# Optimization experiments

Measured on AMD Instinct MI355X. Metric: run time of the kernel, lower is better.

Reference implementation:

```python
import jax, jax.numpy as jnp
import numpy as np

D_MODEL, N_HEADS, D_K, D_V = 1024, 16, 64, 64
B, S = 4, 2048
EPS = 1e-5


def setup_inputs() -> dict:
    key = jax.random.key(0)
    ks = jax.random.split(key, 8)
    scale = 1.0 / np.sqrt(D_MODEL)
    return {
        "input_Q": jax.random.normal(ks[0], (B, S, D_MODEL), dtype=jnp.float32),
        "input_K": jax.random.normal(ks[1], (B, S, D_MODEL), dtype=jnp.float32),
        "input_V": jax.random.normal(ks[2], (B, S, D_MODEL), dtype=jnp.float32),
        "attn_mask": jax.random.bernoulli(ks[3], 0.15, (B, S, S)),  # True = masked
        "W_Q": jax.random.uniform(ks[4], (N_HEADS * D_K, D_MODEL), jnp.float32, -scale, scale),
        "W_K": jax.random.uniform(ks[5], (N_HEADS * D_K, D_MODEL), jnp.float32, -scale, scale),
        "W_V": jax.random.uniform(ks[6], (N_HEADS * D_V, D_MODEL), jnp.float32, -scale, scale),
        "W_fc": jax.random.uniform(ks[7], (D_MODEL, N_HEADS * D_V), jnp.float32, -scale, scale),
    }


def _proj(x, W, h, d):
    # x: [B,S,D] @ W.T ([D, h*d]) -> [B,h,S,d]
    b, s, _ = x.shape
    y = jnp.einsum("bsd,ed->bse", x, W)
    return y.reshape(b, s, h, d).transpose(0, 2, 1, 3)


def reference(input_Q, input_K, input_V, attn_mask, W_Q, W_K, W_V, W_fc):
    b, s, d_model = input_Q.shape
    Q = _proj(input_Q, W_Q, N_HEADS, D_K)  # [B,H,S,dk]
    K = _proj(input_K, W_K, N_HEADS, D_K)
    V = _proj(input_V, W_V, N_HEADS, D_V)

    scores = jnp.einsum("bhqd,bhkd->bhqk", Q, K) / np.sqrt(D_K).astype(np.float32)
    scores = jnp.where(attn_mask[:, None, :, :], jnp.float32(-1e9), scores)
    attn = jax.nn.softmax(scores, axis=-1)  # [B,H,S,S]

    context = jnp.einsum("bhqk,bhkd->bhqd", attn, V)
    context = context.transpose(0, 2, 1, 3).reshape(b, s, N_HEADS * D_V)
    output = jnp.einsum("bse,de->bsd", context, W_fc)

    x = output + input_Q  # residual
    mu = jnp.mean(x, axis=-1, keepdims=True)
    var = jnp.mean(jnp.square(x - mu), axis=-1, keepdims=True)
    ln = (x - mu) / jnp.sqrt(var + EPS)  # fresh LayerNorm: gamma=1, beta=0
    return ln, attn
```

## Files before the change

### kernel.cpp

```cpp
#include <hip/hip_runtime.h>
#include <cstdint>
#include <cstddef>

constexpr int Bc  = 4;
constexpr int Sc  = 2048;
constexpr int DMc = 1024;
constexpr int Hc  = 16;
constexpr int DHc = 64;
constexpr int BHc = Bc * Hc;

typedef float f32x4  __attribute__((ext_vector_type(4)));
typedef short bf16x8 __attribute__((ext_vector_type(8)));

static __device__ __forceinline__ short f2bf(float x) {
  uint32_t u = __builtin_bit_cast(uint32_t, x);
  u += 0x7fffu + ((u >> 16) & 1u);
  return (short)(u >> 16);
}

static __device__ __forceinline__ f32x4 mfma16(bf16x8 a, bf16x8 b, f32x4 c) {
  return __builtin_amdgcn_mfma_f32_16x16x32_bf16(a, b, c, 0, 0, 0);
}

static __device__ __forceinline__ void gload16(const short* g, short* l) {
  __builtin_amdgcn_global_load_lds(
      (const __attribute__((address_space(1))) void*)g,
      (__attribute__((address_space(3))) void*)l, 16, 0, 0);
}

__global__ __launch_bounds__(256) void k_cvtall(const float* __restrict__ iQ,
                                                const float* __restrict__ iK,
                                                const float* __restrict__ iV,
                                                const float* __restrict__ wQ,
                                                const float* __restrict__ wK,
                                                const float* __restrict__ wV,
                                                const float* __restrict__ wO,
                                                short* __restrict__ oQ,
                                                short* __restrict__ oK,
                                                short* __restrict__ oV,
                                                short* __restrict__ owQ,
                                                short* __restrict__ owK,
                                                short* __restrict__ owV,
                                                short* __restrict__ owO) {
  const int bid = blockIdx.x;
  const float* in;
  short* out;
  int ib;
  if (bid < 8192)        { in = iQ; out = oQ; ib = bid; }
  else if (bid < 16384)  { in = iK; out = oK; ib = bid - 8192; }
  else if (bid < 24576)  { in = iV; out = oV; ib = bid - 16384; }
  else {
    const int wb = bid - 24576;
    const int sel = wb >> 10;
    in  = sel == 0 ? wQ : (sel == 1 ? wK : (sel == 2 ? wV : wO));
    out = sel == 0 ? owQ : (sel == 1 ? owK : (sel == 2 ? owV : owO));
    ib = wb & 1023;
  }
  const int i = ib * 256 + threadIdx.x;
  float4 v = reinterpret_cast<const float4*>(in)[i];
  short4 o;
  o.x = f2bf(v.x); o.y = f2bf(v.y); o.z = f2bf(v.z); o.w = f2bf(v.w);
  reinterpret_cast<short4*>(out)[i] = o;
}

template <int MODE>
static __device__ __forceinline__ void gemm_body(const short* __restrict__ A,
                                                 const short* __restrict__ Bt,
                                                 void* __restrict__ out,
                                                 int bm, int bn) {
  __shared__ __align__(16) short lA[128 * 64];
  __shared__ __align__(16) short lB[128 * 64];
  const int tid = threadIdx.x;
  const int lane = tid & 63, w = tid >> 6;
  const int wr = w >> 1, wc = w & 1;
  const int r = lane & 15, g = lane >> 4;

  const int lrow8 = lane >> 3;
  const int lsl   = lane & 7;

  f32x4 acc[4][4] = {};
  const short* Ab = A + (size_t)bm * DMc;
  const short* Bb = Bt + (size_t)bn * DMc;

  for (int k0 = 0; k0 < DMc; k0 += 64) {
    __syncthreads();
    #pragma unroll
    for (int rnd = 0; rnd < 4; rnd++) {
      const int row = rnd * 32 + w * 8 + lrow8;
      const int slot = lsl ^ (row & 7);
      gload16(Ab + (size_t)row * DMc + k0 + slot * 8, lA + (rnd * 32 + w * 8) * 64);
      gload16(Bb + (size_t)row * DMc + k0 + slot * 8, lB + (rnd * 32 + w * 8) * 64);
    }
    __syncthreads();

    #pragma unroll
    for (int kk = 0; kk < 2; kk++) {
      bf16x8 af[4], bfr[4];
      #pragma unroll
      for (int i = 0; i < 4; i++) {
        const int arow = wr * 64 + i * 16 + r;
        af[i] = *reinterpret_cast<const bf16x8*>(
            lA + arow * 64 + (((kk * 4 + g) ^ (arow & 7)) << 3));
        const int brow = wc * 64 + i * 16 + r;
        bfr[i] = *reinterpret_cast<const bf16x8*>(
            lB + brow * 64 + (((kk * 4 + g) ^ (brow & 7)) << 3));
      }
      #pragma unroll
      for (int i = 0; i < 4; i++)
        #pragma unroll
        for (int n = 0; n < 4; n++) acc[i][n] = mfma16(af[i], bfr[n], acc[i][n]);
    }
  }

  #pragma unroll
  for (int i = 0; i < 4; i++) {
    #pragma unroll
    for (int n = 0; n < 4; n++) {
      const int col = bn + wc * 64 + n * 16 + r;
      #pragma unroll
      for (int j = 0; j < 4; j++) {
        const int m = bm + wr * 64 + i * 16 + g * 4 + j;
        if (MODE == 2) {
          reinterpret_cast<float*>(out)[(size_t)m * DMc + col] = acc[i][n][j];
        } else {
          const int b = m >> 11, s = m & (Sc - 1);
          const int h = col >> 6, d = col & (DHc - 1);
          size_t idx = (MODE == 1)
              ? ((size_t)(b * Hc + h) * DHc + d) * Sc + s
              : ((size_t)(b * Hc + h) * Sc + s) * DHc + d;
          reinterpret_cast<short*>(out)[idx] = f2bf(acc[i][n][j]);
        }
      }
    }
  }
}

__global__ __launch_bounds__(256) void k_gemmQKV_pack(
    const short* __restrict__ XQ, const short* __restrict__ XK,
    const short* __restrict__ XV, const short* __restrict__ WQ,
    const short* __restrict__ WK, const short* __restrict__ WV,
    short* __restrict__ Q, short* __restrict__ K, short* __restrict__ V,
    const int* __restrict__ msk, uint32_t* __restrict__ bits) {
  const int bid = blockIdx.x;
  if (bid < 1536) {
    const int rem = bid & 511;
    const int bm = (rem & 63) * 128, bn = (rem >> 6) * 128;
    const int z = bid >> 9;
    if (z == 0)      gemm_body<0>(XQ, WQ, (void*)Q, bm, bn);
    else if (z == 1) gemm_body<0>(XK, WK, (void*)K, bm, bn);
    else             gemm_body<1>(XV, WV, (void*)V, bm, bn);
  } else {
    const size_t wi = (size_t)(bid - 1536) * 256 + threadIdx.x;
    const uint4* mp = reinterpret_cast<const uint4*>(msk + wi * 32);
    uint32_t word = 0;
    #pragma unroll
    for (int q = 0; q < 8; q++) {
      const uint4 mv = mp[q];
      word |= (mv.x != 0 ? 1u : 0u) << (q * 4 + 0);
      word |= (mv.y != 0 ? 1u : 0u) << (q * 4 + 1);
      word |= (mv.z != 0 ? 1u : 0u) << (q * 4 + 2);
      word |= (mv.w != 0 ? 1u : 0u) << (q * 4 + 3);
    }
    bits[wi] = word;
  }
}

__global__ __launch_bounds__(512, 4) void k_flash2(const short* __restrict__ Qb,
                                                   const short* __restrict__ Kb,
                                                   const short* __restrict__ Vt,
                                                   const uint32_t* __restrict__ pbits,
                                                   short* __restrict__ ctx,
                                                   float* __restrict__ attn) {
  __shared__ __align__(16) short kbuf[2][4096];
  __shared__ __align__(16) short vbuf[2][4096];
  __shared__ __align__(16) short pbuf[8][1024];

  const int lin = blockIdx.x;
  const int bh = (lin & 7) * 8 + (lin >> 7);
  const int qbase = ((lin >> 3) & 15) * 128;
  const int b = bh >> 4, h = bh & 15;
  const int tid = threadIdx.x;
  const int lane = tid & 63, w = tid >> 6;
  const int r = lane & 15, g = lane >> 4;
  const int rx = r & 7;

  const int srow = tid >> 3;
  const int sslot = (tid & 7) ^ (srow & 7);
  const short* ksrc = Kb + ((size_t)bh * Sc + srow) * DHc + sslot * 8;
  const short* vsrc = Vt + ((size_t)bh * DHc + srow) * Sc + sslot * 8;
  short* const kdst0 = &kbuf[0][w * 512];
  short* const kdst1 = &kbuf[1][w * 512];
  short* const vdst0 = &vbuf[0][w * 512];
  short* const vdst1 = &vbuf[1][w * 512];

  const short* qrow = Qb + ((size_t)bh * Sc + qbase + w * 16 + r) * DHc;
  const bf16x8 qf0 = *reinterpret_cast<const bf16x8*>(qrow + g * 8);
  const bf16x8 qf1 = *reinterpret_cast<const bf16x8*>(qrow + g * 8 + 32);

  const uint32_t* mrow = pbits + ((size_t)b * Sc + qbase + w * 16 + r) * (Sc / 32);

  constexpr float SCL = 0.18033688f;
  f32x4 pacc[4] = {};
  float rs = 0.f;

  gload16(ksrc, kdst0);
  gload16(vsrc, vdst0);
  __syncthreads();

  int cur = 0;
  for (int kt = 0; kt < 32; kt++) {
    if (kt + 1 < 32) {
      gload16(ksrc + (size_t)(kt + 1) * 64 * DHc, cur ? kdst0 : kdst1);
      gload16(vsrc + (kt + 1) * 64,               cur ? vdst0 : vdst1);
    }
    const short* kb = kbuf[cur];
    const short* vb = vbuf[cur];

    f32x4 sc4[4];
    #pragma unroll
    for (int tt = 0; tt < 4; tt++) {
      const int krow = (tt * 16 + r) * 64;
      bf16x8 kf0 = *reinterpret_cast<const bf16x8*>(kb + krow + ((g ^ rx) << 3));
      bf16x8 kf1 = *reinterpret_cast<const bf16x8*>(kb + krow + (((g + 4) ^ rx) << 3));
      f32x4 a = {};
      a = mfma16(kf0, qf0, a);
      a = mfma16(kf1, qf1, a);
      sc4[tt] = a;
    }

    const uint2 mu = *reinterpret_cast<const uint2*>(mrow + kt * 2);
    #pragma unroll
    for (int tt = 0; tt < 4; tt++) {
      const uint32_t mword = (tt < 2) ? mu.x : mu.y;
      const int bsh = (tt & 1) * 16 + g * 4;
      f32x4 e;
      #pragma unroll
      for (int j = 0; j < 4; j++) {
        float v = __builtin_exp2f(sc4[tt][j] * SCL);
        if ((mword >> (bsh + j)) & 1u) v = 0.f;
        e[j] = v;
        rs += v;
      }
      uint32_t lo = (uint32_t)(uint16_t)f2bf(e[0]) | ((uint32_t)(uint16_t)f2bf(e[1]) << 16);
      uint32_t hi = (uint32_t)(uint16_t)f2bf(e[2]) | ((uint32_t)(uint16_t)f2bf(e[3]) << 16);
      uint64_t pk = (uint64_t)lo | ((uint64_t)hi << 32);
      *reinterpret_cast<uint64_t*>(
          &pbuf[w][r * 64 + (((tt * 2 + (g >> 1)) ^ rx) << 3) + ((g & 1) << 2)]) = pk;
    }

    #pragma unroll
    for (int kt2 = 0; kt2 < 2; kt2++) {
      const int sl = ((kt2 * 4 + g) ^ rx) << 3;
      const bf16x8 paf = *reinterpret_cast<const bf16x8*>(&pbuf[w][r * 64 + sl]);
      #pragma unroll
      for (int n = 0; n < 4; n++) {
        const bf16x8 vf = *reinterpret_cast<const bf16x8*>(vb + (n * 16 + r) * 64 + sl);
        pacc[n] = mfma16(paf, vf, pacc[n]);
      }
    }

    __syncthreads();
    cur ^= 1;
  }

  rs += __shfl_xor(rs, 16);
  rs += __shfl_xor(rs, 32);
  const float rinv = 1.0f / rs;

  float riv[4];
  #pragma unroll
  for (int j = 0; j < 4; j++) riv[j] = 1.0f / __shfl(rs, g * 4 + j);

  short* cbase = ctx + ((size_t)b * Sc + qbase + w * 16) * DMc + h * DHc;
  #pragma unroll
  for (int n = 0; n < 4; n++)
    #pragma unroll
    for (int j = 0; j < 4; j++)
      cbase[(size_t)(g * 4 + j) * DMc + n * 16 + r] = f2bf(pacc[n][j] * riv[j]);

  const short* kbase = Kb + (size_t)bh * Sc * DHc;
  float* out = attn + ((size_t)bh * Sc + qbase + w * 16 + r) * Sc;
  #pragma unroll 2
  for (int kt = 0; kt < 32; kt++) {
    const uint2 mu = *reinterpret_cast<const uint2*>(mrow + kt * 2);
    #pragma unroll
    for (int tt = 0; tt < 4; tt++) {
      const short* krow = kbase + (size_t)(kt * 64 + tt * 16 + r) * DHc;
      bf16x8 kf0 = *reinterpret_cast<const bf16x8*>(krow + g * 8);
      bf16x8 kf1 = *reinterpret_cast<const bf16x8*>(krow + g * 8 + 32);
      f32x4 a = {};
      a = mfma16(kf0, qf0, a);
      a = mfma16(kf1, qf1, a);
      const uint32_t mword = (tt < 2) ? mu.x : mu.y;
      const int bsh = (tt & 1) * 16 + g * 4;
      f32x4 o;
      #pragma unroll
      for (int j = 0; j < 4; j++) {
        float v = __builtin_exp2f(a[j] * SCL) * rinv;
        if ((mword >> (bsh + j)) & 1u) v = 0.f;
        o[j] = v;
      }
      __builtin_nontemporal_store(
          o, reinterpret_cast<f32x4*>(out + kt * 64 + tt * 16 + g * 4));
    }
  }
}

__global__ __launch_bounds__(256) void k_gemmO(const short* __restrict__ A,
                                               const short* __restrict__ Bt,
                                               float* __restrict__ out) {
  gemm_body<2>(A, Bt, (void*)out, blockIdx.x * 128, blockIdx.y * 128);
}

__global__ __launch_bounds__(256) void k_ln(const float* __restrict__ y,
                                            const float* __restrict__ resid,
                                            float* __restrict__ out) {
  const int m = blockIdx.x, t = threadIdx.x;
  const float4 a = reinterpret_cast<const float4*>(y + (size_t)m * DMc)[t];
  const float4 b = reinterpret_cast<const float4*>(resid + (size_t)m * DMc)[t];
  float x0 = a.x + b.x, x1 = a.y + b.y, x2 = a.z + b.z, x3 = a.w + b.w;

  float s = x0 + x1 + x2 + x3;
  #pragma unroll
  for (int m2 = 1; m2 < 64; m2 <<= 1) s += __shfl_xor(s, m2);
  __shared__ float red[4];
  __shared__ float red2[4];
  const int w = t >> 6, lane = t & 63;
  if (lane == 0) red[w] = s;
  __syncthreads();
  const float mean = (red[0] + red[1] + red[2] + red[3]) * (1.0f / DMc);

  x0 -= mean; x1 -= mean; x2 -= mean; x3 -= mean;
  float s2 = x0 * x0 + x1 * x1 + x2 * x2 + x3 * x3;
  #pragma unroll
  for (int m2 = 1; m2 < 64; m2 <<= 1) s2 += __shfl_xor(s2, m2);
  if (lane == 0) red2[w] = s2;
  __syncthreads();
  const float var = (red2[0] + red2[1] + red2[2] + red2[3]) * (1.0f / DMc);
  const float rstd = rsqrtf(var + 1e-5f);

  float4 o;
  o.x = x0 * rstd; o.y = x1 * rstd; o.z = x2 * rstd; o.w = x3 * rstd;
  reinterpret_cast<float4*>(out + (size_t)m * DMc)[t] = o;
}

extern "C" void kernel_launch(void* const* d_in, const int* in_sizes, int n_in,
                              void* d_out, int out_size, void* d_ws, size_t ws_size,
                              hipStream_t stream) {
  const float* inQ = (const float*)d_in[0];
  const float* inK = (const float*)d_in[1];
  const float* inV = (const float*)d_in[2];
  const int*   msk = (const int*)d_in[3];
  const float* WQ  = (const float*)d_in[4];
  const float* WK  = (const float*)d_in[5];
  const float* WV  = (const float*)d_in[6];
  const float* Wfc = (const float*)d_in[7];

  float* out_ln   = (float*)d_out;
  float* out_attn = out_ln + (size_t)Bc * Sc * DMc;

  const size_t NX = (size_t)Bc * Sc * DMc;
  const size_t NW = (size_t)DMc * DMc;
  short* ws = (short*)d_ws;
  short* XbQ = ws;
  short* XbK = XbQ + NX;
  short* XbV = XbK + NX;
  short* WQb = XbV + NX;
  short* WKb = WQb + NW;
  short* WVb = WKb + NW;
  short* Wfb = WVb + NW;
  short* Qb  = Wfb + NW;
  short* Kb  = Qb + NX;
  short* Vt  = Kb + NX;
  uint32_t* pbits = (uint32_t*)(Vt + NX);
  short* ctx = XbV;
  float* y   = (float*)XbQ;

  k_cvtall<<<dim3(28672), 256, 0, stream>>>(inQ, inK, inV, WQ, WK, WV, Wfc,
                                            XbQ, XbK, XbV, WQb, WKb, WVb, Wfb);

  k_gemmQKV_pack<<<dim3(1536 + 2048), 256, 0, stream>>>(
      XbQ, XbK, XbV, WQb, WKb, WVb, Qb, Kb, Vt, msk, pbits);

  k_flash2<<<dim3(1024), 512, 0, stream>>>(Qb, Kb, Vt, pbits, ctx, out_attn);

  k_gemmO<<<dim3(Bc * Sc / 128, DMc / 128), 256, 0, stream>>>(ctx, Wfb, y);

  k_ln<<<dim3(Bc * Sc), 256, 0, stream>>>(y, inQ, out_ln);
}
```

Before: 547.3 us.

## Process two query tiles per block, fusing tile A's attn write with tile B's softmax pass

Each flash block now handles two 128-row query tiles in three phases: row-sum for tile A, then a fused pass that accumulates tile B's softmax-PV while recomputing and writing tile A's normalized attention, then tile B's attention write. K tiles for the write passes now come through the double-buffered LDS pipeline rather than being read directly from global memory. The aim is to share K/V staging across two passes and overlap the heavy attention-matrix store with MFMA work. The cost is half as many blocks (512), which may reduce latency hiding or load balance, plus higher register pressure from holding two Q fragments and two score sets.

```diff
diff --git a/kernel.cpp b/kernel.cpp
--- a/kernel.cpp
+++ b/kernel.cpp
@@ -176,8 +176,9 @@
   __shared__ __align__(16) short pbuf[8][1024];
 
   const int lin = blockIdx.x;
-  const int bh = (lin & 7) * 8 + (lin >> 7);
-  const int qbase = ((lin >> 3) & 15) * 128;
+  const int bh = (lin & 7) * 8 + ((lin >> 3) & 7);
+  const int qA = (lin >> 6) * 256;
+  const int qB = qA + 128;
   const int b = bh >> 4, h = bh & 15;
   const int tid = threadIdx.x;
   const int lane = tid & 63, w = tid >> 6;
@@ -188,30 +189,31 @@
   const int sslot = (tid & 7) ^ (srow & 7);
   const short* ksrc = Kb + ((size_t)bh * Sc + srow) * DHc + sslot * 8;
   const short* vsrc = Vt + ((size_t)bh * DHc + srow) * Sc + sslot * 8;
-  short* const kdst0 = &kbuf[0][w * 512];
-  short* const kdst1 = &kbuf[1][w * 512];
-  short* const vdst0 = &vbuf[0][w * 512];
-  short* const vdst1 = &vbuf[1][w * 512];
-
-  const short* qrow = Qb + ((size_t)bh * Sc + qbase + w * 16 + r) * DHc;
-  const bf16x8 qf0 = *reinterpret_cast<const bf16x8*>(qrow + g * 8);
-  const bf16x8 qf1 = *reinterpret_cast<const bf16x8*>(qrow + g * 8 + 32);
-
-  const uint32_t* mrow = pbits + ((size_t)b * Sc + qbase + w * 16 + r) * (Sc / 32);
+  short* const kdst[2] = {&kbuf[0][w * 512], &kbuf[1][w * 512]};
+  short* const vdst[2] = {&vbuf[0][w * 512], &vbuf[1][w * 512]};
+
+  const short* qrowA = Qb + ((size_t)bh * Sc + qA + w * 16 + r) * DHc;
+  const bf16x8 qfA0 = *reinterpret_cast<const bf16x8*>(qrowA + g * 8);
+  const bf16x8 qfA1 = *reinterpret_cast<const bf16x8*>(qrowA + g * 8 + 32);
+  const short* qrowB = Qb + ((size_t)bh * Sc + qB + w * 16 + r) * DHc;
+  const bf16x8 qfB0 = *reinterpret_cast<const bf16x8*>(qrowB + g * 8);
+  const bf16x8 qfB1 = *reinterpret_cast<const bf16x8*>(qrowB + g * 8 + 32);
+
+  const uint32_t* mrowA = pbits + ((size_t)b * Sc + qA + w * 16 + r) * (Sc / 32);
+  const uint32_t* mrowB = pbits + ((size_t)b * Sc + qB + w * 16 + r) * (Sc / 32);
 
   constexpr float SCL = 0.18033688f;
   f32x4 pacc[4] = {};
   float rs = 0.f;
 
-  gload16(ksrc, kdst0);
-  gload16(vsrc, vdst0);
+  gload16(ksrc, kdst[0]);
+  gload16(vsrc, vdst[0]);
   __syncthreads();
-
   int cur = 0;
   for (int kt = 0; kt < 32; kt++) {
     if (kt + 1 < 32) {
-      gload16(ksrc + (size_t)(kt + 1) * 64 * DHc, cur ? kdst0 : kdst1);
-      gload16(vsrc + (kt + 1) * 64,               cur ? vdst0 : vdst1);
+      gload16(ksrc + (size_t)(kt + 1) * 64 * DHc, kdst[cur ^ 1]);
+      gload16(vsrc + (kt + 1) * 64,               vdst[cur ^ 1]);
     }
     const short* kb = kbuf[cur];
     const short* vb = vbuf[cur];
@@ -223,12 +225,12 @@
       bf16x8 kf0 = *reinterpret_cast<const bf16x8*>(kb + krow + ((g ^ rx) << 3));
       bf16x8 kf1 = *reinterpret_cast<const bf16x8*>(kb + krow + (((g + 4) ^ rx) << 3));
       f32x4 a = {};
-      a = mfma16(kf0, qf0, a);
-      a = mfma16(kf1, qf1, a);
+      a = mfma16(kf0, qfA0, a);
+      a = mfma16(kf1, qfA1, a);
       sc4[tt] = a;
     }
 
-    const uint2 mu = *reinterpret_cast<const uint2*>(mrow + kt * 2);
+    const uint2 mu = *reinterpret_cast<const uint2*>(mrowA + kt * 2);
     #pragma unroll
     for (int tt = 0; tt < 4; tt++) {
       const uint32_t mword = (tt < 2) ? mu.x : mu.y;
@@ -249,8 +251,8 @@
     }
 
     #pragma unroll
-    for (int kt2 = 0; kt2 < 2; kt2++) {
-      const int sl = ((kt2 * 4 + g) ^ rx) << 3;
+    for (int kk = 0; kk < 2; kk++) {
+      const int sl = ((kk * 4 + g) ^ rx) << 3;
       const bf16x8 paf = *reinterpret_cast<const bf16x8*>(&pbuf[w][r * 64 + sl]);
       #pragma unroll
       for (int n = 0; n < 4; n++) {
@@ -258,51 +260,152 @@
         pacc[n] = mfma16(paf, vf, pacc[n]);
       }
     }
-
     __syncthreads();
     cur ^= 1;
   }
 
   rs += __shfl_xor(rs, 16);
   rs += __shfl_xor(rs, 32);
-  const float rinv = 1.0f / rs;
-
-  float riv[4];
+  const float rinvA = 1.0f / rs;
+  {
+    float riv[4];
+    #pragma unroll
+    for (int j = 0; j < 4; j++) riv[j] = 1.0f / __shfl(rs, g * 4 + j);
+    short* cbase = ctx + ((size_t)b * Sc + qA + w * 16) * DMc + h * DHc;
+    #pragma unroll
+    for (int n = 0; n < 4; n++)
+      #pragma unroll
+      for (int j = 0; j < 4; j++)
+        cbase[(size_t)(g * 4 + j) * DMc + n * 16 + r] = f2bf(pacc[n][j] * riv[j]);
+  }
+
   #pragma unroll
-  for (int j = 0; j < 4; j++) riv[j] = 1.0f / __shfl(rs, g * 4 + j);
-
-  short* cbase = ctx + ((size_t)b * Sc + qbase + w * 16) * DMc + h * DHc;
-  #pragma unroll
-  for (int n = 0; n < 4; n++)
-    #pragma unroll
-    for (int j = 0; j < 4; j++)
-      cbase[(size_t)(g * 4 + j) * DMc + n * 16 + r] = f2bf(pacc[n][j] * riv[j]);
-
-  const short* kbase = Kb + (size_t)bh * Sc * DHc;
-  float* out = attn + ((size_t)bh * Sc + qbase + w * 16 + r) * Sc;
-  #pragma unroll 2
+  for (int n = 0; n < 4; n++) pacc[n] = f32x4{};
+  rs = 0.f;
+  float* outA = attn + ((size_t)bh * Sc + qA + w * 16 + r) * Sc;
+
+  gload16(ksrc, kdst[cur]);
+  gload16(vsrc, vdst[cur]);
+  __syncthreads();
   for (int kt = 0; kt < 32; kt++) {
-    const uint2 mu = *reinterpret_cast<const uint2*>(mrow + kt * 2);
+    if (kt + 1 < 32) {
+      gload16(ksrc + (size_t)(kt + 1) * 64 * DHc, kdst[cur ^ 1]);
+      gload16(vsrc + (kt + 1) * 64,               vdst[cur ^ 1]);
+    }
+    const short* kb = kbuf[cur];
+    const short* vb = vbuf[cur];
+
+    f32x4 scB[4], scA[4];
     #pragma unroll
     for (int tt = 0; tt < 4; tt++) {
-      const short* krow = kbase + (size_t)(kt * 64 + tt * 16 + r) * DHc;
-      bf16x8 kf0 = *reinterpret_cast<const bf16x8*>(krow + g * 8);
-      bf16x8 kf1 = *reinterpret_cast<const bf16x8*>(krow + g * 8 + 32);
+      const int krow = (tt * 16 + r) * 64;
+      bf16x8 kf0 = *reinterpret_cast<const bf16x8*>(kb + krow + ((g ^ rx) << 3));
+      bf16x8 kf1 = *reinterpret_cast<const bf16x8*>(kb + krow + (((g + 4) ^ rx) << 3));
       f32x4 a = {};
-      a = mfma16(kf0, qf0, a);
-      a = mfma16(kf1, qf1, a);
+      a = mfma16(kf0, qfB0, a);
+      a = mfma16(kf1, qfB1, a);
+      scB[tt] = a;
+      f32x4 c = {};
+      c = mfma16(kf0, qfA0, c);
+      c = mfma16(kf1, qfA1, c);
+      scA[tt] = c;
+    }
+
+    const uint2 muB = *reinterpret_cast<const uint2*>(mrowB + kt * 2);
+    const uint2 muA = *reinterpret_cast<const uint2*>(mrowA + kt * 2);
+    #pragma unroll
+    for (int tt = 0; tt < 4; tt++) {
+      const int bsh = (tt & 1) * 16 + g * 4;
+      {
+        const uint32_t mword = (tt < 2) ? muB.x : muB.y;
+        f32x4 e;
+        #pragma unroll
+        for (int j = 0; j < 4; j++) {
+          float v = __builtin_exp2f(scB[tt][j] * SCL);
+          if ((mword >> (bsh + j)) & 1u) v = 0.f;
+          e[j] = v;
+          rs += v;
+        }
+        uint32_t lo = (uint32_t)(uint16_t)f2bf(e[0]) | ((uint32_t)(uint16_t)f2bf(e[1]) << 16);
+        uint32_t hi = (uint32_t)(uint16_t)f2bf(e[2]) | ((uint32_t)(uint16_t)f2bf(e[3]) << 16);
+        uint64_t pk = (uint64_t)lo | ((uint64_t)hi << 32);
+        *reinterpret_cast<uint64_t*>(
+            &pbuf[w][r * 64 + (((tt * 2 + (g >> 1)) ^ rx) << 3) + ((g & 1) << 2)]) = pk;
+      }
+      {
+        const uint32_t mword = (tt < 2) ? muA.x : muA.y;
+        f32x4 o;
+        #pragma unroll
+        for (int j = 0; j < 4; j++) {
+          float v = __builtin_exp2f(scA[tt][j] * SCL) * rinvA;
+          if ((mword >> (bsh + j)) & 1u) v = 0.f;
+          o[j] = v;
+        }
+        __builtin_nontemporal_store(
+            o, reinterpret_cast<f32x4*>(outA + kt * 64 + tt * 16 + g * 4));
+      }
+    }
+
+    #pragma unroll
+    for (int kk = 0; kk < 2; kk++) {
+      const int sl = ((kk * 4 + g) ^ rx) << 3;
+      const bf16x8 paf = *reinterpret_cast<const bf16x8*>(&pbuf[w][r * 64 + sl]);
+      #pragma unroll
+      for (int n = 0; n < 4; n++) {
+        const bf16x8 vf = *reinterpret_cast<const bf16x8*>(vb + (n * 16 + r) * 64 + sl);
+        pacc[n] = mfma16(paf, vf, pacc[n]);
+      }
+    }
+    __syncthreads();
+    cur ^= 1;
+  }
+
+  rs += __shfl_xor(rs, 16);
+  rs += __shfl_xor(rs, 32);
+  const float rinvB = 1.0f / rs;
+  {
+    float riv[4];
+    #pragma unroll
+    for (int j = 0; j < 4; j++) riv[j] = 1.0f / __shfl(rs, g * 4 + j);
+    short* cbase = ctx + ((size_t)b * Sc + qB + w * 16) * DMc + h * DHc;
+    #pragma unroll
+    for (int n = 0; n < 4; n++)
+      #pragma unroll
+      for (int j = 0; j < 4; j++)
+        cbase[(size_t)(g * 4 + j) * DMc + n * 16 + r] = f2bf(pacc[n][j] * riv[j]);
+  }
+
+  float* outB = attn + ((size_t)bh * Sc + qB + w * 16 + r) * Sc;
+  gload16(ksrc, kdst[cur]);
+  __syncthreads();
+  for (int kt = 0; kt < 32; kt++) {
+    if (kt + 1 < 32)
+      gload16(ksrc + (size_t)(kt + 1) * 64 * DHc, kdst[cur ^ 1]);
+    const short* kb = kbuf[cur];
+
+    const uint2 mu = *reinterpret_cast<const uint2*>(mrowB + kt * 2);
+    #pragma unroll
+    for (int tt = 0; tt < 4; tt++) {
+      const int krow = (tt * 16 + r) * 64;
+      bf16x8 kf0 = *reinterpret_cast<const bf16x8*>(kb + krow + ((g ^ rx) << 3));
+      bf16x8 kf1 = *reinterpret_cast<const bf16x8*>(kb + krow + (((g + 4) ^ rx) << 3));
+      f32x4 a = {};
+      a = mfma16(kf0, qfB0, a);
+      a = mfma16(kf1, qfB1, a);
       const uint32_t mword = (tt < 2) ? mu.x : mu.y;
       const int bsh = (tt & 1) * 16 + g * 4;
       f32x4 o;
       #pragma unroll
       for (int j = 0; j < 4; j++) {
-        float v = __builtin_exp2f(a[j] * SCL) * rinv;
+        float v = __builtin_exp2f(a[j] * SCL) * rinvB;
         if ((mword >> (bsh + j)) & 1u) v = 0.f;
         o[j] = v;
       }
       __builtin_nontemporal_store(
-          o, reinterpret_cast<f32x4*>(out + kt * 64 + tt * 16 + g * 4));
-    }
+          o, reinterpret_cast<f32x4*>(outB + kt * 64 + tt * 16 + g * 4));
+    }
+    __syncthreads();
+    cur ^= 1;
   }
 }
 
@@ -382,7 +485,7 @@
   k_gemmQKV_pack<<<dim3(1536 + 2048), 256, 0, stream>>>(
       XbQ, XbK, XbV, WQb, WKb, WVb, Qb, Kb, Vt, msk, pbits);
 
-  k_flash2<<<dim3(1024), 512, 0, stream>>>(Qb, Kb, Vt, pbits, ctx, out_attn);
+  k_flash2<<<dim3(512), 512, 0, stream>>>(Qb, Kb, Vt, pbits, ctx, out_attn);
 
   k_gemmO<<<dim3(Bc * Sc / 128, DMc / 128), 256, 0, stream>>>(ctx, Wfb, y);
 
```

Result: slower. 639.3 us (+16.8%).
